# Optimization experiments

Hardware: AMD Instinct MI355X
Metric: run time of the kernel (lower is better)

## Reference

```python
import jax, jax.numpy as jnp
import numpy as np

N_NODES = 100000


def gcn_conv(x, src, dst, w, W, b, n):
    """PyG GCNConv: out = D^{-1/2} (A+I) D^{-1/2} (x @ W) + b (self-loops weight 1)."""
    loop = jnp.arange(n, dtype=src.dtype)
    s = jnp.concatenate([src, loop])
    d = jnp.concatenate([dst, loop])
    ew = jnp.concatenate([w, jnp.ones((n,), x.dtype)])
    deg = jax.ops.segment_sum(ew, d, num_segments=n)            # degree of target nodes
    dinv = jnp.where(deg > 0, jax.lax.rsqrt(deg), jnp.zeros_like(deg))
    norm = dinv[s] * ew * dinv[d]                               # [E+N]
    h = x @ W                                                   # [N, out] dense transform first
    msg = h[s] * norm[:, None]                                  # gather + scale
    out = jax.ops.segment_sum(msg, d, num_segments=n)           # scatter-add aggregate
    return out + b


def setup_inputs() -> dict:
    key = jax.random.key(0)
    k1, k2, k3, k4, k5, k6 = jax.random.split(key, 6)
    in_dim, hid, out_dim = 128, 128, 64
    n_edges = 1600000
    x = jax.random.normal(k1, (N_NODES, in_dim), dtype=jnp.float32)
    edge_index = jax.random.randint(k2, (2, n_edges), 0, N_NODES, dtype=jnp.int32)
    edge_weight = jax.random.uniform(k3, (n_edges,), dtype=jnp.float32)
    # Glorot-style weights, zero bias (as in GCNConv defaults)
    W1 = jax.random.normal(k4, (in_dim, hid), dtype=jnp.float32) / np.sqrt(in_dim)
    b1 = jnp.zeros((hid,), jnp.float32)
    W2 = jax.random.normal(k5, (hid, out_dim), dtype=jnp.float32) / np.sqrt(hid)
    b2 = jnp.zeros((out_dim,), jnp.float32)
    return {"x": x, "edge_index": edge_index, "edge_weight": edge_weight,
            "W1": W1, "b1": b1, "W2": W2, "b2": b2}


def reference(x, edge_index, edge_weight, W1, b1, W2, b2):
    src, dst = edge_index[0], edge_index[1]
    h = gcn_conv(x, src, dst, edge_weight, W1, b1, N_NODES)
    h = jax.nn.relu(h)
    # dropout is identity in eval mode
    out = gcn_conv(h, src, dst, edge_weight, W2, b2, N_NODES)
    return out
```

## Files before the change

### kernel.cpp

```cpp
#include <hip/hip_runtime.h>
#include <cstdint>
#include <cstddef>


typedef unsigned long long u64;
typedef unsigned int u32;
typedef unsigned short u16;
typedef __attribute__((ext_vector_type(8))) short bf16x8;
typedef __attribute__((ext_vector_type(4))) float f32x4;

__device__ __forceinline__ float bflo(u32 u) { return __uint_as_float(u << 16); }
__device__ __forceinline__ float bfhi(u32 u) { return __uint_as_float(u & 0xffff0000u); }
__device__ __forceinline__ u32 f2bf(float f) {
  u32 u = __float_as_uint(f);
  return (u + 0x7fffu + ((u >> 16) & 1u)) >> 16;
}
__device__ __forceinline__ u32 pack2bf(float lo, float hi) {
  return f2bf(lo) | (f2bf(hi) << 16);
}

__global__ void degrank_kernel(const int* __restrict__ dst, const float* __restrict__ w,
                               u64* packed, u16* __restrict__ rank, int E) {
  int e = blockIdx.x * 256 + threadIdx.x;
  if (e < E) {
    int d = dst[e];
    u64 add = (1ull << 48) | (u64)(w[e] * 4294967296.0f);
    u64 old = atomicAdd(&packed[d], add);
    rank[e] = (u16)(old >> 48);
  }
}

__global__ __launch_bounds__(256) void gemm1_kernel(const float* __restrict__ x,
                                                    const float* __restrict__ W1,
                                                    u16* __restrict__ h1, int M) {
  __shared__ u16 Wt[128][136];
  const int tid = threadIdx.x;
  for (int i = tid; i < 128 * 128; i += 256) {
    int c = i >> 7, k = i & 127;
    Wt[c][k] = (u16)f2bf(W1[(size_t)k * 128 + c]);
  }
  __syncthreads();

  const int wv = tid >> 6;
  const int l = tid & 63;
  const int c16 = l & 15;
  const int kg = l >> 4;
  const int arow = blockIdx.x * 64 + wv * 16 + c16;
  const bool rok = arow < M;

  bf16x8 ahi[4], alo[4];
  #pragma unroll
  for (int kk = 0; kk < 4; ++kk) {
    float v[8];
    if (rok) {
      float4 p0 = *reinterpret_cast<const float4*>(x + (size_t)arow * 128 + kk * 32 + kg * 8);
      float4 p1 = *reinterpret_cast<const float4*>(x + (size_t)arow * 128 + kk * 32 + kg * 8 + 4);
      v[0] = p0.x; v[1] = p0.y; v[2] = p0.z; v[3] = p0.w;
      v[4] = p1.x; v[5] = p1.y; v[6] = p1.z; v[7] = p1.w;
    } else {
      #pragma unroll
      for (int j = 0; j < 8; ++j) v[j] = 0.f;
    }
    #pragma unroll
    for (int j = 0; j < 8; ++j) {
      u32 hb = f2bf(v[j]);
      float hf = __uint_as_float(hb << 16);
      u32 lb = f2bf(v[j] - hf);
      ahi[kk][j] = (short)hb;
      alo[kk][j] = (short)lb;
    }
  }

  #pragma unroll
  for (int ct = 0; ct < 8; ++ct) {
    f32x4 acc = {0.f, 0.f, 0.f, 0.f};
    #pragma unroll
    for (int kk = 0; kk < 4; ++kk) {
      bf16x8 b = *reinterpret_cast<const bf16x8*>(&Wt[ct * 16 + c16][kk * 32 + kg * 8]);
      acc = __builtin_amdgcn_mfma_f32_16x16x32_bf16(alo[kk], b, acc, 0, 0, 0);
      acc = __builtin_amdgcn_mfma_f32_16x16x32_bf16(ahi[kk], b, acc, 0, 0, 0);
    }
    #pragma unroll
    for (int r = 0; r < 4; ++r) {
      int gr = blockIdx.x * 64 + wv * 16 + kg * 4 + r;
      if (gr < M) h1[(size_t)gr * 128 + ct * 16 + c16] = (u16)f2bf(acc[r]);
    }
  }
}

__global__ void scan_kernel(const u64* __restrict__ packed, int* __restrict__ rowstart,
                            int* __restrict__ bsum, int* __restrict__ boff,
                            u32* __restrict__ counter, float* __restrict__ dinvp,
                            int n, int nblk) {
  __shared__ int wsum[4];
  __shared__ bool amLast;
  int b = blockIdx.x;
  int base = b * 1024;
  int tid = threadIdx.x;
  int lane = tid & 63, wv = tid >> 6;
  int idx = base + tid * 4;
  int v0 = 0, v1 = 0, v2 = 0, v3 = 0;
  #pragma unroll
  for (int j = 0; j < 4; ++j) {
    if (idx + j < n) {
      u64 p = packed[idx + j];
      int c = (int)(p >> 48);
      if (j == 0) v0 = c; else if (j == 1) v1 = c; else if (j == 2) v2 = c; else v3 = c;
      float deg = 1.0f + (float)((double)(p & 0xFFFFFFFFFFFFull) * 2.3283064365386963e-10);
      dinvp[idx + j] = rsqrtf(deg);
    }
  }
  int tsum = v0 + v1 + v2 + v3;
  int inc = tsum;
  #pragma unroll
  for (int off = 1; off < 64; off <<= 1) {
    int u = __shfl_up(inc, off, 64);
    if (lane >= off) inc += u;
  }
  if (lane == 63) wsum[wv] = inc;
  __syncthreads();
  int woff = 0;
  for (int w2 = 0; w2 < wv; ++w2) woff += wsum[w2];
  int texc = woff + inc - tsum;
  if (idx     < n) rowstart[idx]     = texc;
  if (idx + 1 < n) rowstart[idx + 1] = texc + v0;
  if (idx + 2 < n) rowstart[idx + 2] = texc + v0 + v1;
  if (idx + 3 < n) rowstart[idx + 3] = texc + v0 + v1 + v2;
  if (tid == 255) {
    bsum[b] = woff + inc;
    if (b == nblk - 1) rowstart[n] = woff + inc;
  }
  __threadfence();
  if (tid == 0) amLast = (atomicAdd(counter, 1u) == (u32)(nblk - 1));
  __syncthreads();
  if (amLast) {
    __threadfence();
    int v = (tid < nblk) ? bsum[tid] : 0;
    int inc2 = v;
    #pragma unroll
    for (int off = 1; off < 64; off <<= 1) {
      int u = __shfl_up(inc2, off, 64);
      if (lane >= off) inc2 += u;
    }
    if (lane == 63) wsum[wv] = inc2;
    __syncthreads();
    int woff2 = 0;
    for (int w2 = 0; w2 < wv; ++w2) woff2 += wsum[w2];
    if (tid < nblk) boff[tid] = woff2 + inc2 - v;
  }
}

__global__ void fill_kernel(const int* __restrict__ src, const int* __restrict__ dst,
                            const float* __restrict__ w, const u16* __restrict__ rank,
                            const float* __restrict__ dinv, const int* __restrict__ rowstart,
                            const int* __restrict__ boff, int2* __restrict__ erec, int E) {
  int e = blockIdx.x * 256 + threadIdx.x;
  if (e < E) {
    int s = src[e], d = dst[e];
    int pos = rowstart[d] + boff[d >> 10] + (int)rank[e];
    float nrm = dinv[s] * w[e] * dinv[d];
    erec[pos] = make_int2(s, __float_as_int(nrm));
  }
}

__global__ __launch_bounds__(256) void gemm2_kernel(const u16* __restrict__ A,
                                                    const float* __restrict__ W2,
                                                    u16* __restrict__ C, int M) {
  __shared__ u16 Wt[64][136];
  const int tid = threadIdx.x;
  for (int i = tid; i < 128 * 64; i += 256) {
    int c = i >> 7, k = i & 127;
    Wt[c][k] = (u16)f2bf(W2[(size_t)k * 64 + c]);
  }
  __syncthreads();

  const int wv = tid >> 6;
  const int l = tid & 63;
  const int c16 = l & 15;
  const int kg = l >> 4;
  const int arow = blockIdx.x * 64 + wv * 16 + c16;
  const bool rok = arow < M;

  bf16x8 af[4];
  #pragma unroll
  for (int kk = 0; kk < 4; ++kk) {
    if (rok) {
      af[kk] = *reinterpret_cast<const bf16x8*>(A + (size_t)arow * 128 + kk * 32 + kg * 8);
    } else {
      af[kk] = bf16x8{0, 0, 0, 0, 0, 0, 0, 0};
    }
  }

  #pragma unroll
  for (int ct = 0; ct < 4; ++ct) {
    f32x4 acc = {0.f, 0.f, 0.f, 0.f};
    #pragma unroll
    for (int kk = 0; kk < 4; ++kk) {
      bf16x8 b = *reinterpret_cast<const bf16x8*>(&Wt[ct * 16 + c16][kk * 32 + kg * 8]);
      acc = __builtin_amdgcn_mfma_f32_16x16x32_bf16(af[kk], b, acc, 0, 0, 0);
    }
    #pragma unroll
    for (int r = 0; r < 4; ++r) {
      int gr = blockIdx.x * 64 + wv * 16 + kg * 4 + r;
      if (gr < M) C[(size_t)gr * 64 + ct * 16 + c16] = (u16)f2bf(acc[r]);
    }
  }
}

__global__ __launch_bounds__(256) void agg128_relu_kernel(
    const uint2* __restrict__ H2, const int* __restrict__ rowstart,
    const int* __restrict__ boff, const int2* __restrict__ erec,
    const float* __restrict__ dinv, const float* __restrict__ bias,
    uint2* __restrict__ out2, int n) {
  int wid = (blockIdx.x * 256 + threadIdx.x) >> 6;
  int lane = threadIdx.x & 63;
  int node = wid * 2 + (lane >> 5);
  int hl = lane & 31;
  if (node >= n) return;
  float dv = dinv[node];
  float ns = dv * dv;
  uint2 hv = H2[(size_t)node * 32 + hl];
  float a0 = ns * bflo(hv.x), a1 = ns * bfhi(hv.x);
  float a2 = ns * bflo(hv.y), a3 = ns * bfhi(hv.y);
  int e  = rowstart[node] + boff[node >> 10];
  int e1 = rowstart[node + 1] + boff[(node + 1) >> 10];
  for (; e + 7 < e1; e += 8) {
    int2 r0 = erec[e], r1 = erec[e + 1], r2 = erec[e + 2], r3 = erec[e + 3];
    int2 r4 = erec[e + 4], r5 = erec[e + 5], r6 = erec[e + 6], r7 = erec[e + 7];
    uint2 v0 = H2[(size_t)r0.x * 32 + hl];
    uint2 v1 = H2[(size_t)r1.x * 32 + hl];
    uint2 v2 = H2[(size_t)r2.x * 32 + hl];
    uint2 v3 = H2[(size_t)r3.x * 32 + hl];
    uint2 v4 = H2[(size_t)r4.x * 32 + hl];
    uint2 v5 = H2[(size_t)r5.x * 32 + hl];
    uint2 v6 = H2[(size_t)r6.x * 32 + hl];
    uint2 v7 = H2[(size_t)r7.x * 32 + hl];
    float w0 = __int_as_float(r0.y), w1 = __int_as_float(r1.y);
    float w2 = __int_as_float(r2.y), w3 = __int_as_float(r3.y);
    float w4 = __int_as_float(r4.y), w5 = __int_as_float(r5.y);
    float w6 = __int_as_float(r6.y), w7 = __int_as_float(r7.y);
    a0 += w0 * bflo(v0.x) + w1 * bflo(v1.x) + w2 * bflo(v2.x) + w3 * bflo(v3.x)
        + w4 * bflo(v4.x) + w5 * bflo(v5.x) + w6 * bflo(v6.x) + w7 * bflo(v7.x);
    a1 += w0 * bfhi(v0.x) + w1 * bfhi(v1.x) + w2 * bfhi(v2.x) + w3 * bfhi(v3.x)
        + w4 * bfhi(v4.x) + w5 * bfhi(v5.x) + w6 * bfhi(v6.x) + w7 * bfhi(v7.x);
    a2 += w0 * bflo(v0.y) + w1 * bflo(v1.y) + w2 * bflo(v2.y) + w3 * bflo(v3.y)
        + w4 * bflo(v4.y) + w5 * bflo(v5.y) + w6 * bflo(v6.y) + w7 * bflo(v7.y);
    a3 += w0 * bfhi(v0.y) + w1 * bfhi(v1.y) + w2 * bfhi(v2.y) + w3 * bfhi(v3.y)
        + w4 * bfhi(v4.y) + w5 * bfhi(v5.y) + w6 * bfhi(v6.y) + w7 * bfhi(v7.y);
  }
  for (; e + 3 < e1; e += 4) {
    int2 r0 = erec[e], r1 = erec[e + 1], r2 = erec[e + 2], r3 = erec[e + 3];
    uint2 v0 = H2[(size_t)r0.x * 32 + hl];
    uint2 v1 = H2[(size_t)r1.x * 32 + hl];
    uint2 v2 = H2[(size_t)r2.x * 32 + hl];
    uint2 v3 = H2[(size_t)r3.x * 32 + hl];
    float w0 = __int_as_float(r0.y), w1 = __int_as_float(r1.y);
    float w2 = __int_as_float(r2.y), w3 = __int_as_float(r3.y);
    a0 += w0 * bflo(v0.x) + w1 * bflo(v1.x) + w2 * bflo(v2.x) + w3 * bflo(v3.x);
    a1 += w0 * bfhi(v0.x) + w1 * bfhi(v1.x) + w2 * bfhi(v2.x) + w3 * bfhi(v3.x);
    a2 += w0 * bflo(v0.y) + w1 * bflo(v1.y) + w2 * bflo(v2.y) + w3 * bflo(v3.y);
    a3 += w0 * bfhi(v0.y) + w1 * bfhi(v1.y) + w2 * bfhi(v2.y) + w3 * bfhi(v3.y);
  }
  for (; e < e1; ++e) {
    int2 r = erec[e];
    uint2 v = H2[(size_t)r.x * 32 + hl];
    float w = __int_as_float(r.y);
    a0 += w * bflo(v.x); a1 += w * bfhi(v.x);
    a2 += w * bflo(v.y); a3 += w * bfhi(v.y);
  }
  float4 bb = reinterpret_cast<const float4*>(bias)[hl];
  a0 = fmaxf(a0 + bb.x, 0.f);
  a1 = fmaxf(a1 + bb.y, 0.f);
  a2 = fmaxf(a2 + bb.z, 0.f);
  a3 = fmaxf(a3 + bb.w, 0.f);
  out2[(size_t)node * 32 + hl] = make_uint2(pack2bf(a0, a1), pack2bf(a2, a3));
}

__global__ __launch_bounds__(256) void agg64_kernel(
    const u32* __restrict__ H, const int* __restrict__ rowstart,
    const int* __restrict__ boff, const int2* __restrict__ erec,
    const float* __restrict__ dinv, const float* __restrict__ bias,
    float2* __restrict__ out2, int n) {
  int wid = (blockIdx.x * 256 + threadIdx.x) >> 6;
  int lane = threadIdx.x & 63;
  int node = wid * 2 + (lane >> 5);
  int hl = lane & 31;
  if (node >= n) return;
  float dv = dinv[node];
  float ns = dv * dv;
  u32 hv = H[(size_t)node * 32 + hl];
  float a0 = ns * bflo(hv), a1 = ns * bfhi(hv);
  int e  = rowstart[node] + boff[node >> 10];
  int e1 = rowstart[node + 1] + boff[(node + 1) >> 10];
  for (; e + 7 < e1; e += 8) {
    int2 r0 = erec[e], r1 = erec[e + 1], r2 = erec[e + 2], r3 = erec[e + 3];
    int2 r4 = erec[e + 4], r5 = erec[e + 5], r6 = erec[e + 6], r7 = erec[e + 7];
    u32 v0 = H[(size_t)r0.x * 32 + hl];
    u32 v1 = H[(size_t)r1.x * 32 + hl];
    u32 v2 = H[(size_t)r2.x * 32 + hl];
    u32 v3 = H[(size_t)r3.x * 32 + hl];
    u32 v4 = H[(size_t)r4.x * 32 + hl];
    u32 v5 = H[(size_t)r5.x * 32 + hl];
    u32 v6 = H[(size_t)r6.x * 32 + hl];
    u32 v7 = H[(size_t)r7.x * 32 + hl];
    a0 += __int_as_float(r0.y) * bflo(v0) + __int_as_float(r1.y) * bflo(v1)
        + __int_as_float(r2.y) * bflo(v2) + __int_as_float(r3.y) * bflo(v3)
        + __int_as_float(r4.y) * bflo(v4) + __int_as_float(r5.y) * bflo(v5)
        + __int_as_float(r6.y) * bflo(v6) + __int_as_float(r7.y) * bflo(v7);
    a1 += __int_as_float(r0.y) * bfhi(v0) + __int_as_float(r1.y) * bfhi(v1)
        + __int_as_float(r2.y) * bfhi(v2) + __int_as_float(r3.y) * bfhi(v3)
        + __int_as_float(r4.y) * bfhi(v4) + __int_as_float(r5.y) * bfhi(v5)
        + __int_as_float(r6.y) * bfhi(v6) + __int_as_float(r7.y) * bfhi(v7);
  }
  for (; e + 3 < e1; e += 4) {
    int2 r0 = erec[e], r1 = erec[e + 1], r2 = erec[e + 2], r3 = erec[e + 3];
    u32 v0 = H[(size_t)r0.x * 32 + hl];
    u32 v1 = H[(size_t)r1.x * 32 + hl];
    u32 v2 = H[(size_t)r2.x * 32 + hl];
    u32 v3 = H[(size_t)r3.x * 32 + hl];
    a0 += __int_as_float(r0.y) * bflo(v0) + __int_as_float(r1.y) * bflo(v1)
        + __int_as_float(r2.y) * bflo(v2) + __int_as_float(r3.y) * bflo(v3);
    a1 += __int_as_float(r0.y) * bfhi(v0) + __int_as_float(r1.y) * bfhi(v1)
        + __int_as_float(r2.y) * bfhi(v2) + __int_as_float(r3.y) * bfhi(v3);
  }
  for (; e < e1; ++e) {
    int2 r = erec[e];
    u32 v = H[(size_t)r.x * 32 + hl];
    float w = __int_as_float(r.y);
    a0 += w * bflo(v);
    a1 += w * bfhi(v);
  }
  float2 bb = reinterpret_cast<const float2*>(bias)[hl];
  out2[(size_t)node * 32 + hl] = make_float2(a0 + bb.x, a1 + bb.y);
}

extern "C" void kernel_launch(void* const* d_in, const int* in_sizes, int n_in,
                              void* d_out, int out_size, void* d_ws, size_t ws_size,
                              hipStream_t stream) {
  const float* x  = (const float*)d_in[0];
  const int*   ei = (const int*)d_in[1];
  const float* ew = (const float*)d_in[2];
  const float* W1 = (const float*)d_in[3];
  const float* b1 = (const float*)d_in[4];
  const float* W2 = (const float*)d_in[5];
  const float* b2 = (const float*)d_in[6];
  float* out = (float*)d_out;
  const int N = in_sizes[0] / 128;
  const int E = in_sizes[2];
  const int* src = ei;
  const int* dst = ei + E;

  char* wsB = (char*)d_ws;
  size_t off = 0;
  auto alloc = [&](size_t bytes) {
    void* p = wsB + off;
    off += ((bytes + 255) / 256) * 256;
    return p;
  };
  u64*   packed  = (u64*)alloc((size_t)N * 8);
  u32*   counter = (u32*)alloc(256);
  float* dinv    = (float*)alloc((size_t)N * 4);
  u16*   rank    = (u16*)alloc((size_t)E * 2);
  int*   rowst   = (int*)alloc((size_t)(N + 1) * 4);
  int*   bsum    = (int*)alloc(256 * 4);
  int*   boff    = (int*)alloc(256 * 4);
  int2*  erec    = (int2*)alloc((size_t)E * 8);
  u16*   h1      = (u16*)alloc((size_t)N * 128 * 2);
  u16*   a1      = (u16*)alloc((size_t)N * 128 * 2);
  u16*   h2      = h1;

  const int eb = (E + 255) / 256;
  const int nbx = (N + 63) / 64;
  const int nblk = (N + 1023) / 1024;

  hipMemsetAsync(d_ws, 0, (size_t)N * 8 + 256, stream);
  degrank_kernel<<<eb, 256, 0, stream>>>(dst, ew, packed, rank, E);
  gemm1_kernel<<<nbx, 256, 0, stream>>>(x, W1, h1, N);
  scan_kernel<<<nblk, 256, 0, stream>>>(packed, rowst, bsum, boff, counter, dinv, N, nblk);
  fill_kernel<<<eb, 256, 0, stream>>>(src, dst, ew, rank, dinv, rowst, boff, erec, E);

  const int ab = (N + 7) / 8;
  agg128_relu_kernel<<<ab, 256, 0, stream>>>((const uint2*)h1, rowst, boff, erec, dinv, b1,
                                             (uint2*)a1, N);
  gemm2_kernel<<<nbx, 256, 0, stream>>>(a1, W2, h2, N);
  agg64_kernel<<<ab, 256, 0, stream>>>((const u32*)h2, rowst, boff, erec, dinv, b2,
                                       (float2*)out, N);
}
```

Measured before the change: 434.7 us.

## Fuse layer-1 aggregation with second GEMM and pack edge records into 32 bits

Merges the layer-1 aggregation/ReLU kernel with the second dense transform, keeping the aggregated rows in shared memory so the intermediate activation matrix is never written to or read back from global memory. Edge records shrink from 8 bytes to 4 by packing a 17-bit source index with a 15-bit fixed-point normalisation weight, halving edge-stream traffic in both aggregations. The 8-way unrolled loops are dropped in favour of 4-way. The quantised weight loses precision, clamps norms at just under 1, and the packing assumes node indices fit in 17 bits.

New measurement: 431.7 us. No clear change (-0.7%).

```diff
diff --git a/kernel.cpp b/kernel.cpp
--- a/kernel.cpp
+++ b/kernel.cpp
@@ -17,6 +17,9 @@
 }
 __device__ __forceinline__ u32 pack2bf(float lo, float hi) {
   return f2bf(lo) | (f2bf(hi) << 16);
+}
+__device__ __forceinline__ float dec_norm(u32 rec) {
+  return (float)(rec & 32767u) * 3.0517578125e-05f;
 }
 
 __global__ void degrank_kernel(const int* __restrict__ dst, const float* __restrict__ w,
@@ -153,132 +156,104 @@
 __global__ void fill_kernel(const int* __restrict__ src, const int* __restrict__ dst,
                             const float* __restrict__ w, const u16* __restrict__ rank,
                             const float* __restrict__ dinv, const int* __restrict__ rowstart,
-                            const int* __restrict__ boff, int2* __restrict__ erec, int E) {
+                            const int* __restrict__ boff, u32* __restrict__ erec, int E) {
   int e = blockIdx.x * 256 + threadIdx.x;
   if (e < E) {
     int s = src[e], d = dst[e];
     int pos = rowstart[d] + boff[d >> 10] + (int)rank[e];
     float nrm = dinv[s] * w[e] * dinv[d];
-    erec[pos] = make_int2(s, __float_as_int(nrm));
-  }
-}
-
-__global__ __launch_bounds__(256) void gemm2_kernel(const u16* __restrict__ A,
-                                                    const float* __restrict__ W2,
-                                                    u16* __restrict__ C, int M) {
+    u32 q = (u32)(nrm * 32768.0f);
+    if (q > 32767u) q = 32767u;
+    erec[pos] = ((u32)s << 15) | q;
+  }
+}
+
+__global__ __launch_bounds__(512) void agg1_gemm2_kernel(
+    const uint2* __restrict__ H2, const int* __restrict__ rowstart,
+    const int* __restrict__ boff, const u32* __restrict__ erec,
+    const float* __restrict__ dinv, const float* __restrict__ b1,
+    const float* __restrict__ W2, u16* __restrict__ h2, int n) {
+  __shared__ u16 A1[64][136];
   __shared__ u16 Wt[64][136];
   const int tid = threadIdx.x;
-  for (int i = tid; i < 128 * 64; i += 256) {
+  const int wave = tid >> 6;
+  const int lane = tid & 63;
+  const int base = blockIdx.x * 64;
+
+  for (int i = tid; i < 64 * 128; i += 512) {
     int c = i >> 7, k = i & 127;
     Wt[c][k] = (u16)f2bf(W2[(size_t)k * 64 + c]);
   }
+
+  const int hl = lane & 31;
+  #pragma unroll
+  for (int p = 0; p < 4; ++p) {
+    int r = wave * 8 + p * 2 + (lane >> 5);
+    int node = base + r;
+    if (node < n) {
+      float dv = dinv[node];
+      float ns = dv * dv;
+      uint2 hv = H2[(size_t)node * 32 + hl];
+      float a0 = ns * bflo(hv.x), a1v = ns * bfhi(hv.x);
+      float a2 = ns * bflo(hv.y), a3 = ns * bfhi(hv.y);
+      int e  = rowstart[node] + boff[node >> 10];
+      int e1 = rowstart[node + 1] + boff[(node + 1) >> 10];
+      for (; e + 3 < e1; e += 4) {
+        u32 r0 = erec[e], r1 = erec[e + 1], r2 = erec[e + 2], r3 = erec[e + 3];
+        uint2 v0 = H2[(size_t)(r0 >> 15) * 32 + hl];
+        uint2 v1 = H2[(size_t)(r1 >> 15) * 32 + hl];
+        uint2 v2 = H2[(size_t)(r2 >> 15) * 32 + hl];
+        uint2 v3 = H2[(size_t)(r3 >> 15) * 32 + hl];
+        float w0 = dec_norm(r0), w1 = dec_norm(r1), w2 = dec_norm(r2), w3 = dec_norm(r3);
+        a0  += w0 * bflo(v0.x) + w1 * bflo(v1.x) + w2 * bflo(v2.x) + w3 * bflo(v3.x);
+        a1v += w0 * bfhi(v0.x) + w1 * bfhi(v1.x) + w2 * bfhi(v2.x) + w3 * bfhi(v3.x);
+        a2  += w0 * bflo(v0.y) + w1 * bflo(v1.y) + w2 * bflo(v2.y) + w3 * bflo(v3.y);
+        a3  += w0 * bfhi(v0.y) + w1 * bfhi(v1.y) + w2 * bfhi(v2.y) + w3 * bfhi(v3.y);
+      }
+      for (; e < e1; ++e) {
+        u32 rr = erec[e];
+        uint2 v = H2[(size_t)(rr >> 15) * 32 + hl];
+        float w = dec_norm(rr);
+        a0 += w * bflo(v.x); a1v += w * bfhi(v.x);
+        a2 += w * bflo(v.y); a3  += w * bfhi(v.y);
+      }
+      float4 bb = reinterpret_cast<const float4*>(b1)[hl];
+      a0  = fmaxf(a0 + bb.x, 0.f);
+      a1v = fmaxf(a1v + bb.y, 0.f);
+      a2  = fmaxf(a2 + bb.z, 0.f);
+      a3  = fmaxf(a3 + bb.w, 0.f);
+      *reinterpret_cast<uint2*>(&A1[r][hl * 4]) =
+          make_uint2(pack2bf(a0, a1v), pack2bf(a2, a3));
+    } else {
+      *reinterpret_cast<uint2*>(&A1[r][hl * 4]) = make_uint2(0u, 0u);
+    }
+  }
   __syncthreads();
 
-  const int wv = tid >> 6;
-  const int l = tid & 63;
-  const int c16 = l & 15;
-  const int kg = l >> 4;
-  const int arow = blockIdx.x * 64 + wv * 16 + c16;
-  const bool rok = arow < M;
-
-  bf16x8 af[4];
-  #pragma unroll
-  for (int kk = 0; kk < 4; ++kk) {
-    if (rok) {
-      af[kk] = *reinterpret_cast<const bf16x8*>(A + (size_t)arow * 128 + kk * 32 + kg * 8);
-    } else {
-      af[kk] = bf16x8{0, 0, 0, 0, 0, 0, 0, 0};
-    }
-  }
-
-  #pragma unroll
-  for (int ct = 0; ct < 4; ++ct) {
+  const int c16 = lane & 15;
+  const int kg = lane >> 4;
+  #pragma unroll
+  for (int t = wave * 2; t < wave * 2 + 2; ++t) {
+    int rt = t >> 2;
+    int ctile = t & 3;
     f32x4 acc = {0.f, 0.f, 0.f, 0.f};
     #pragma unroll
     for (int kk = 0; kk < 4; ++kk) {
-      bf16x8 b = *reinterpret_cast<const bf16x8*>(&Wt[ct * 16 + c16][kk * 32 + kg * 8]);
-      acc = __builtin_amdgcn_mfma_f32_16x16x32_bf16(af[kk], b, acc, 0, 0, 0);
+      bf16x8 a = *reinterpret_cast<const bf16x8*>(&A1[rt * 16 + c16][kk * 32 + kg * 8]);
+      bf16x8 b = *reinterpret_cast<const bf16x8*>(&Wt[ctile * 16 + c16][kk * 32 + kg * 8]);
+      acc = __builtin_amdgcn_mfma_f32_16x16x32_bf16(a, b, acc, 0, 0, 0);
     }
     #pragma unroll
     for (int r = 0; r < 4; ++r) {
-      int gr = blockIdx.x * 64 + wv * 16 + kg * 4 + r;
-      if (gr < M) C[(size_t)gr * 64 + ct * 16 + c16] = (u16)f2bf(acc[r]);
-    }
-  }
-}
-
-__global__ __launch_bounds__(256) void agg128_relu_kernel(
-    const uint2* __restrict__ H2, const int* __restrict__ rowstart,
-    const int* __restrict__ boff, const int2* __restrict__ erec,
-    const float* __restrict__ dinv, const float* __restrict__ bias,
-    uint2* __restrict__ out2, int n) {
-  int wid = (blockIdx.x * 256 + threadIdx.x) >> 6;
-  int lane = threadIdx.x & 63;
-  int node = wid * 2 + (lane >> 5);
-  int hl = lane & 31;
-  if (node >= n) return;
-  float dv = dinv[node];
-  float ns = dv * dv;
-  uint2 hv = H2[(size_t)node * 32 + hl];
-  float a0 = ns * bflo(hv.x), a1 = ns * bfhi(hv.x);
-  float a2 = ns * bflo(hv.y), a3 = ns * bfhi(hv.y);
-  int e  = rowstart[node] + boff[node >> 10];
-  int e1 = rowstart[node + 1] + boff[(node + 1) >> 10];
-  for (; e + 7 < e1; e += 8) {
-    int2 r0 = erec[e], r1 = erec[e + 1], r2 = erec[e + 2], r3 = erec[e + 3];
-    int2 r4 = erec[e + 4], r5 = erec[e + 5], r6 = erec[e + 6], r7 = erec[e + 7];
-    uint2 v0 = H2[(size_t)r0.x * 32 + hl];
-    uint2 v1 = H2[(size_t)r1.x * 32 + hl];
-    uint2 v2 = H2[(size_t)r2.x * 32 + hl];
-    uint2 v3 = H2[(size_t)r3.x * 32 + hl];
-    uint2 v4 = H2[(size_t)r4.x * 32 + hl];
-    uint2 v5 = H2[(size_t)r5.x * 32 + hl];
-    uint2 v6 = H2[(size_t)r6.x * 32 + hl];
-    uint2 v7 = H2[(size_t)r7.x * 32 + hl];
-    float w0 = __int_as_float(r0.y), w1 = __int_as_float(r1.y);
-    float w2 = __int_as_float(r2.y), w3 = __int_as_float(r3.y);
-    float w4 = __int_as_float(r4.y), w5 = __int_as_float(r5.y);
-    float w6 = __int_as_float(r6.y), w7 = __int_as_float(r7.y);
-    a0 += w0 * bflo(v0.x) + w1 * bflo(v1.x) + w2 * bflo(v2.x) + w3 * bflo(v3.x)
-        + w4 * bflo(v4.x) + w5 * bflo(v5.x) + w6 * bflo(v6.x) + w7 * bflo(v7.x);
-    a1 += w0 * bfhi(v0.x) + w1 * bfhi(v1.x) + w2 * bfhi(v2.x) + w3 * bfhi(v3.x)
-        + w4 * bfhi(v4.x) + w5 * bfhi(v5.x) + w6 * bfhi(v6.x) + w7 * bfhi(v7.x);
-    a2 += w0 * bflo(v0.y) + w1 * bflo(v1.y) + w2 * bflo(v2.y) + w3 * bflo(v3.y)
-        + w4 * bflo(v4.y) + w5 * bflo(v5.y) + w6 * bflo(v6.y) + w7 * bflo(v7.y);
-    a3 += w0 * bfhi(v0.y) + w1 * bfhi(v1.y) + w2 * bfhi(v2.y) + w3 * bfhi(v3.y)
-        + w4 * bfhi(v4.y) + w5 * bfhi(v5.y) + w6 * bfhi(v6.y) + w7 * bfhi(v7.y);
-  }
-  for (; e + 3 < e1; e += 4) {
-    int2 r0 = erec[e], r1 = erec[e + 1], r2 = erec[e + 2], r3 = erec[e + 3];
-    uint2 v0 = H2[(size_t)r0.x * 32 + hl];
-    uint2 v1 = H2[(size_t)r1.x * 32 + hl];
-    uint2 v2 = H2[(size_t)r2.x * 32 + hl];
-    uint2 v3 = H2[(size_t)r3.x * 32 + hl];
-    float w0 = __int_as_float(r0.y), w1 = __int_as_float(r1.y);
-    float w2 = __int_as_float(r2.y), w3 = __int_as_float(r3.y);
-    a0 += w0 * bflo(v0.x) + w1 * bflo(v1.x) + w2 * bflo(v2.x) + w3 * bflo(v3.x);
-    a1 += w0 * bfhi(v0.x) + w1 * bfhi(v1.x) + w2 * bfhi(v2.x) + w3 * bfhi(v3.x);
-    a2 += w0 * bflo(v0.y) + w1 * bflo(v1.y) + w2 * bflo(v2.y) + w3 * bflo(v3.y);
-    a3 += w0 * bfhi(v0.y) + w1 * bfhi(v1.y) + w2 * bfhi(v2.y) + w3 * bfhi(v3.y);
-  }
-  for (; e < e1; ++e) {
-    int2 r = erec[e];
-    uint2 v = H2[(size_t)r.x * 32 + hl];
-    float w = __int_as_float(r.y);
-    a0 += w * bflo(v.x); a1 += w * bfhi(v.x);
-    a2 += w * bflo(v.y); a3 += w * bfhi(v.y);
-  }
-  float4 bb = reinterpret_cast<const float4*>(bias)[hl];
-  a0 = fmaxf(a0 + bb.x, 0.f);
-  a1 = fmaxf(a1 + bb.y, 0.f);
-  a2 = fmaxf(a2 + bb.z, 0.f);
-  a3 = fmaxf(a3 + bb.w, 0.f);
-  out2[(size_t)node * 32 + hl] = make_uint2(pack2bf(a0, a1), pack2bf(a2, a3));
+      int grow = base + rt * 16 + kg * 4 + r;
+      if (grow < n) h2[(size_t)grow * 64 + ctile * 16 + c16] = (u16)f2bf(acc[r]);
+    }
+  }
 }
 
 __global__ __launch_bounds__(256) void agg64_kernel(
     const u32* __restrict__ H, const int* __restrict__ rowstart,
-    const int* __restrict__ boff, const int2* __restrict__ erec,
+    const int* __restrict__ boff, const u32* __restrict__ erec,
     const float* __restrict__ dinv, const float* __restrict__ bias,
     float2* __restrict__ out2, int n) {
   int wid = (blockIdx.x * 256 + threadIdx.x) >> 6;
@@ -292,41 +267,20 @@
   float a0 = ns * bflo(hv), a1 = ns * bfhi(hv);
   int e  = rowstart[node] + boff[node >> 10];
   int e1 = rowstart[node + 1] + boff[(node + 1) >> 10];
-  for (; e + 7 < e1; e += 8) {
-    int2 r0 = erec[e], r1 = erec[e + 1], r2 = erec[e + 2], r3 = erec[e + 3];
-    int2 r4 = erec[e + 4], r5 = erec[e + 5], r6 = erec[e + 6], r7 = erec[e + 7];
-    u32 v0 = H[(size_t)r0.x * 32 + hl];
-    u32 v1 = H[(size_t)r1.x * 32 + hl];
-    u32 v2 = H[(size_t)r2.x * 32 + hl];
-    u32 v3 = H[(size_t)r3.x * 32 + hl];
-    u32 v4 = H[(size_t)r4.x * 32 + hl];
-    u32 v5 = H[(size_t)r5.x * 32 + hl];
-    u32 v6 = H[(size_t)r6.x * 32 + hl];
-    u32 v7 = H[(size_t)r7.x * 32 + hl];
-    a0 += __int_as_float(r0.y) * bflo(v0) + __int_as_float(r1.y) * bflo(v1)
-        + __int_as_float(r2.y) * bflo(v2) + __int_as_float(r3.y) * bflo(v3)
-        + __int_as_float(r4.y) * bflo(v4) + __int_as_float(r5.y) * bflo(v5)
-        + __int_as_float(r6.y) * bflo(v6) + __int_as_float(r7.y) * bflo(v7);
-    a1 += __int_as_float(r0.y) * bfhi(v0) + __int_as_float(r1.y) * bfhi(v1)
-        + __int_as_float(r2.y) * bfhi(v2) + __int_as_float(r3.y) * bfhi(v3)
-        + __int_as_float(r4.y) * bfhi(v4) + __int_as_float(r5.y) * bfhi(v5)
-        + __int_as_float(r6.y) * bfhi(v6) + __int_as_float(r7.y) * bfhi(v7);
-  }
   for (; e + 3 < e1; e += 4) {
-    int2 r0 = erec[e], r1 = erec[e + 1], r2 = erec[e + 2], r3 = erec[e + 3];
-    u32 v0 = H[(size_t)r0.x * 32 + hl];
-    u32 v1 = H[(size_t)r1.x * 32 + hl];
-    u32 v2 = H[(size_t)r2.x * 32 + hl];
-    u32 v3 = H[(size_t)r3.x * 32 + hl];
-    a0 += __int_as_float(r0.y) * bflo(v0) + __int_as_float(r1.y) * bflo(v1)
-        + __int_as_float(r2.y) * bflo(v2) + __int_as_float(r3.y) * bflo(v3);
-    a1 += __int_as_float(r0.y) * bfhi(v0) + __int_as_float(r1.y) * bfhi(v1)
-        + __int_as_float(r2.y) * bfhi(v2) + __int_as_float(r3.y) * bfhi(v3);
+    u32 r0 = erec[e], r1 = erec[e + 1], r2 = erec[e + 2], r3 = erec[e + 3];
+    u32 v0 = H[(size_t)(r0 >> 15) * 32 + hl];
+    u32 v1 = H[(size_t)(r1 >> 15) * 32 + hl];
+    u32 v2 = H[(size_t)(r2 >> 15) * 32 + hl];
+    u32 v3 = H[(size_t)(r3 >> 15) * 32 + hl];
+    float w0 = dec_norm(r0), w1 = dec_norm(r1), w2 = dec_norm(r2), w3 = dec_norm(r3);
+    a0 += w0 * bflo(v0) + w1 * bflo(v1) + w2 * bflo(v2) + w3 * bflo(v3);
+    a1 += w0 * bfhi(v0) + w1 * bfhi(v1) + w2 * bfhi(v2) + w3 * bfhi(v3);
   }
   for (; e < e1; ++e) {
-    int2 r = erec[e];
-    u32 v = H[(size_t)r.x * 32 + hl];
-    float w = __int_as_float(r.y);
+    u32 rr = erec[e];
+    u32 v = H[(size_t)(rr >> 15) * 32 + hl];
+    float w = dec_norm(rr);
     a0 += w * bflo(v);
     a1 += w * bfhi(v);
   }
@@ -364,10 +318,9 @@
   int*   rowst   = (int*)alloc((size_t)(N + 1) * 4);
   int*   bsum    = (int*)alloc(256 * 4);
   int*   boff    = (int*)alloc(256 * 4);
-  int2*  erec    = (int2*)alloc((size_t)E * 8);
+  u32*   erec    = (u32*)alloc((size_t)E * 4);
   u16*   h1      = (u16*)alloc((size_t)N * 128 * 2);
-  u16*   a1      = (u16*)alloc((size_t)N * 128 * 2);
-  u16*   h2      = h1;
+  u16*   h2      = (u16*)alloc((size_t)N * 64 * 2);
 
   const int eb = (E + 255) / 256;
   const int nbx = (N + 63) / 64;
@@ -379,10 +332,9 @@
   scan_kernel<<<nblk, 256, 0, stream>>>(packed, rowst, bsum, boff, counter, dinv, N, nblk);
   fill_kernel<<<eb, 256, 0, stream>>>(src, dst, ew, rank, dinv, rowst, boff, erec, E);
 
+  agg1_gemm2_kernel<<<nbx, 512, 0, stream>>>((const uint2*)h1, rowst, boff, erec, dinv,
+                                             b1, W2, h2, N);
   const int ab = (N + 7) / 8;
-  agg128_relu_kernel<<<ab, 256, 0, stream>>>((const uint2*)h1, rowst, boff, erec, dinv, b1,
-                                             (uint2*)a1, N);
-  gemm2_kernel<<<nbx, 256, 0, stream>>>(a1, W2, h2, N);
   agg64_kernel<<<ab, 256, 0, stream>>>((const u32*)h2, rowst, boff, erec, dinv, b2,
                                        (float2*)out, N);
 }
```
